# Kernel tuning notes

Hardware: AMD Instinct MI355X
Metric: run time of the kernel (lower is better)

Reference implementation:

```python
import jax, jax.numpy as jnp
import numpy as np

B, R, T, D = 16, 1024, 512, 1024
H = 1024  # hidden_dim

def setup_inputs() -> dict:
    key = jax.random.key(0)
    ks = jax.random.split(key, 8)
    s_in = 1.0 / np.sqrt(D)
    s_comb = 1.0 / np.sqrt(3 * D)
    return {
        "region_feats": jax.random.normal(ks[0], (B, R, D), jnp.float32),
        "query_embs": jax.random.normal(ks[1], (B, T, D), jnp.float32),
        "Wr": jax.random.normal(ks[2], (D, H), jnp.float32) * s_in,
        "br": jnp.zeros((H,), jnp.float32),
        "Wq": jax.random.normal(ks[3], (D, H), jnp.float32) * s_in,
        "bq": jnp.zeros((H,), jnp.float32),
        "Ws": jax.random.normal(ks[4], (3 * D, 1), jnp.float32) * s_comb,
        "bs": jnp.zeros((1,), jnp.float32),
    }

def reference(region_feats, query_embs, Wr, br, Wq, bq, Ws, bs):
    # Dense projections
    R_proj = region_feats @ Wr + br            # [B,R,H]
    Q_proj = query_embs @ Wq + bq              # [B,T,H]
    # Unscaled cross-attention scores
    scores = jnp.einsum('brd,btd->brt', R_proj, Q_proj)  # [B,R,T]
    attn = jax.nn.softmax(scores, axis=-1)
    # Attend over RAW query embeddings (as in source)
    attended = jnp.einsum('brt,btd->brd', attn, query_embs)  # [B,R,D]
    combined = jnp.concatenate(
        [region_feats, attended, region_feats * attended], axis=-1)  # [B,R,3D]
    out = combined @ Ws + bs                    # [B,R,1]
    return jnp.squeeze(out, axis=-1)            # [B,R]
```

## Files before the change

kernel.cpp:

```cpp
#include <hip/hip_runtime.h>


#define BD 16
#define RD 1024
#define TD 512
#define DD 1024
#define BR (BD * RD)

typedef _Float16 half8 __attribute__((ext_vector_type(8)));
typedef _Float16 half4 __attribute__((ext_vector_type(4)));
typedef float floatx4 __attribute__((ext_vector_type(4)));

__device__ __forceinline__ float wave_sum(float v) {
#pragma unroll
  for (int off = 32; off > 0; off >>= 1) v += __shfl_down(v, off);
  return v;
}

template <bool FUSED>
__global__ __launch_bounds__(256) void gemm_pipe(
    const _Float16* __restrict__ A, const _Float16* __restrict__ B0,
    const _Float16* __restrict__ B1, _Float16* __restrict__ C,
    float* __restrict__ Ms, float* __restrict__ Ls, float* __restrict__ Hs,
    const float* __restrict__ cvec, const _Float16* __restrict__ wsh,
    int N, int K, long sA, long sB, long sC) {
  constexpr int TT = FUSED ? 3 : 2;
  __shared__ __align__(16) _Float16 lds[2 * TT * 4096];
  __shared__ __align__(16) _Float16 wlds[FUSED ? 2048 : 16];

  const int b = blockIdx.z;
  A += (long)b * sA;
  B0 += (long)b * sB;
  if (FUSED) B1 += (long)b * sB;
  const int m0 = blockIdx.y * 128, n0 = blockIdx.x * 128;
  const int tid = threadIdx.x, lane = tid & 63, w = tid >> 6;
  const int wr = w >> 1, wc = w & 1;

  const int srow = lane >> 2;
  const int slot = lane & 3;
  const int scol = (slot ^ ((srow >> 1) & 3)) * 8;
  const _Float16* gA = A + (long)(m0 + 32 * w + srow) * K + scol;
  const _Float16* gP = B0 + (long)(n0 + 32 * w + srow) * K + scol;
  const _Float16* gQ = FUSED ? B1 + (long)(n0 + 32 * w + srow) * K + scol : nullptr;
  const long rstep = (long)16 * K;
  const int wofs = (32 * w + srow) * 32 + slot * 8;

  if (FUSED) *(int4*)&wlds[tid * 8] = *(const int4*)&wsh[tid * 8];

  const int NK = K / 32;
  int4 pA0, pA1, pP0, pP1, pQ0, pQ1;
  pA0 = *(const int4*)gA;
  pA1 = *(const int4*)(gA + rstep);
  pP0 = *(const int4*)gP;
  pP1 = *(const int4*)(gP + rstep);
  if (FUSED) {
    pQ0 = *(const int4*)gQ;
    pQ1 = *(const int4*)(gQ + rstep);
  }
  *(int4*)&lds[wofs] = pA0;
  *(int4*)&lds[wofs + 512] = pA1;
  *(int4*)&lds[4096 + wofs] = pP0;
  *(int4*)&lds[4096 + wofs + 512] = pP1;
  if (FUSED) {
    *(int4*)&lds[8192 + wofs] = pQ0;
    *(int4*)&lds[8192 + wofs + 512] = pQ1;
  }
  if (NK > 1) {
    pA0 = *(const int4*)(gA + 32);
    pA1 = *(const int4*)(gA + rstep + 32);
    pP0 = *(const int4*)(gP + 32);
    pP1 = *(const int4*)(gP + rstep + 32);
    if (FUSED) {
      pQ0 = *(const int4*)(gQ + 32);
      pQ1 = *(const int4*)(gQ + rstep + 32);
    }
  }
  __syncthreads();

  floatx4 accS[4][4] = {};
  floatx4 accH[4][4] = {};
  const int fr = lane & 15, g = lane >> 4;
  const int fs = (g ^ ((fr >> 1) & 3)) * 8;

  for (int kt = 0; kt < NK; ++kt) {
    const int cur = (kt & 1) * TT * 4096;
    const int nxt = ((kt + 1) & 1) * TT * 4096;
    if (kt + 1 < NK) {
      *(int4*)&lds[nxt + wofs] = pA0;
      *(int4*)&lds[nxt + wofs + 512] = pA1;
      *(int4*)&lds[nxt + 4096 + wofs] = pP0;
      *(int4*)&lds[nxt + 4096 + wofs + 512] = pP1;
      if (FUSED) {
        *(int4*)&lds[nxt + 8192 + wofs] = pQ0;
        *(int4*)&lds[nxt + 8192 + wofs + 512] = pQ1;
      }
    }
    if (kt + 2 < NK) {
      const long go = (long)(kt + 2) * 32;
      pA0 = *(const int4*)(gA + go);
      pA1 = *(const int4*)(gA + rstep + go);
      pP0 = *(const int4*)(gP + go);
      pP1 = *(const int4*)(gP + rstep + go);
      if (FUSED) {
        pQ0 = *(const int4*)(gQ + go);
        pQ1 = *(const int4*)(gQ + rstep + go);
      }
    }
    half8 af[4], bp[4], bq[4], w1f, w2f;
#pragma unroll
    for (int i = 0; i < 4; ++i)
      af[i] = *(const half8*)&lds[cur + (64 * wr + 16 * i + fr) * 32 + fs];
#pragma unroll
    for (int j = 0; j < 4; ++j)
      bp[j] = *(const half8*)&lds[cur + 4096 + (64 * wc + 16 * j + fr) * 32 + fs];
    if (FUSED) {
#pragma unroll
      for (int j = 0; j < 4; ++j)
        bq[j] = *(const half8*)&lds[cur + 8192 + (64 * wc + 16 * j + fr) * 32 + fs];
      w1f = *(const half8*)&wlds[kt * 32 + g * 8];
      w2f = *(const half8*)&wlds[1024 + kt * 32 + g * 8];
    }
#pragma unroll
    for (int i = 0; i < 4; ++i)
#pragma unroll
      for (int j = 0; j < 4; ++j)
        accS[i][j] = __builtin_amdgcn_mfma_f32_16x16x32_f16(af[i], bp[j], accS[i][j], 0, 0, 0);
    if (FUSED) {
#pragma unroll
      for (int i = 0; i < 4; ++i) af[i] = w1f + af[i] * w2f;
#pragma unroll
      for (int i = 0; i < 4; ++i)
#pragma unroll
        for (int j = 0; j < 4; ++j)
          accH[i][j] = __builtin_amdgcn_mfma_f32_16x16x32_f16(af[i], bq[j], accH[i][j], 0, 0, 0);
    }
    __syncthreads();
  }

  const int cr = g * 4, cc = fr;
  if (!FUSED) {
    _Float16* Cw = C + (long)b * sC;
#pragma unroll
    for (int i = 0; i < 4; ++i)
#pragma unroll
      for (int r = 0; r < 4; ++r)
#pragma unroll
        for (int j = 0; j < 4; ++j)
          Cw[(long)(m0 + 64 * wr + 16 * i + cr + r) * N + n0 + 64 * wc + 16 * j + cc] =
              (_Float16)accS[i][j][r];
  } else {
    float cv[4];
#pragma unroll
    for (int j = 0; j < 4; ++j)
      cv[j] = cvec[(long)b * TD + n0 + 64 * wc + 16 * j + cc];
    const int chunk = blockIdx.x * 2 + wc;
    const long rowBase = (long)b * RD + m0 + 64 * wr + cr;
#pragma unroll
    for (int i = 0; i < 4; ++i) {
#pragma unroll
      for (int r = 0; r < 4; ++r) {
        float mx = -1e30f;
#pragma unroll
        for (int j = 0; j < 4; ++j) mx = fmaxf(mx, accS[i][j][r] + cv[j]);
        mx = fmaxf(mx, __shfl_xor(mx, 1));
        mx = fmaxf(mx, __shfl_xor(mx, 2));
        mx = fmaxf(mx, __shfl_xor(mx, 4));
        mx = fmaxf(mx, __shfl_xor(mx, 8));
        float l = 0.f, hs = 0.f;
#pragma unroll
        for (int j = 0; j < 4; ++j) {
          const float e = __expf(accS[i][j][r] + cv[j] - mx);
          l += e;
          hs += e * accH[i][j][r];
        }
        l += __shfl_xor(l, 1); hs += __shfl_xor(hs, 1);
        l += __shfl_xor(l, 2); hs += __shfl_xor(hs, 2);
        l += __shfl_xor(l, 4); hs += __shfl_xor(hs, 4);
        l += __shfl_xor(l, 8); hs += __shfl_xor(hs, 8);
        if (cc == 0) {
          const long idx = (long)chunk * BR + rowBase + 16 * i + r;
          Ms[idx] = mx;
          Ls[idx] = l;
          Hs[idx] = hs;
        }
      }
    }
  }
}

__global__ __launch_bounds__(256) void combine(
    const float* __restrict__ Ms, const float* __restrict__ Ls,
    const float* __restrict__ Hs, const float* __restrict__ rdvec,
    const float* __restrict__ bs, float* __restrict__ out) {
  const int row = blockIdx.x * 256 + threadIdx.x;
  float mv[8];
  float gm = -1e30f;
#pragma unroll
  for (int c = 0; c < 8; ++c) {
    mv[c] = Ms[(long)c * BR + row];
    gm = fmaxf(gm, mv[c]);
  }
  float L = 0.f, HS = 0.f;
#pragma unroll
  for (int c = 0; c < 8; ++c) {
    const float s = __expf(mv[c] - gm);
    L += Ls[(long)c * BR + row] * s;
    HS += Hs[(long)c * BR + row] * s;
  }
  out[row] = HS / L + rdvec[row] + bs[0];
}

__global__ __launch_bounds__(256) void cvt_f2h(const float* __restrict__ in,
                                               _Float16* __restrict__ out) {
  const long i = ((long)blockIdx.x * 256 + threadIdx.x) * 4;
  const float4 v = *(const float4*)&in[i];
  half4 h = {(_Float16)v.x, (_Float16)v.y, (_Float16)v.z, (_Float16)v.w};
  *(half4*)&out[i] = h;
}

__global__ __launch_bounds__(256) void conv_region(
    const float* __restrict__ region, const float* __restrict__ Ws,
    _Float16* __restrict__ r16, float* __restrict__ rdvec) {
  const long row = blockIdx.x;
  const int tid = threadIdx.x, lane = tid & 63, wid = tid >> 6;
  const long i = row * DD + tid * 4;
  const float4 v = *(const float4*)&region[i];
  half4 h = {(_Float16)v.x, (_Float16)v.y, (_Float16)v.z, (_Float16)v.w};
  *(half4*)&r16[i] = h;
  const float4 w0 = *(const float4*)&Ws[tid * 4];
  float rd = v.x * w0.x + v.y * w0.y + v.z * w0.z + v.w * w0.w;
  rd = wave_sum(rd);
  __shared__ float sm[4];
  if (lane == 0) sm[wid] = rd;
  __syncthreads();
  if (tid == 0) rdvec[row] = sm[0] + sm[1] + sm[2] + sm[3];
}

__global__ __launch_bounds__(256) void conv_query(
    const float* __restrict__ query, const float* __restrict__ wqbr,
    _Float16* __restrict__ q16, float* __restrict__ cvec) {
  const long row = blockIdx.x;
  const int tid = threadIdx.x, lane = tid & 63, wid = tid >> 6;
  const long i = row * DD + tid * 4;
  const float4 v = *(const float4*)&query[i];
  half4 h = {(_Float16)v.x, (_Float16)v.y, (_Float16)v.z, (_Float16)v.w};
  *(half4*)&q16[i] = h;
  const float4 w = *(const float4*)&wqbr[tid * 4];
  float c = v.x * w.x + v.y * w.y + v.z * w.z + v.w * w.w;
  c = wave_sum(c);
  __shared__ float sm[4];
  if (lane == 0) sm[wid] = c;
  __syncthreads();
  if (tid == 0) cvec[row] = sm[0] + sm[1] + sm[2] + sm[3];
}

__global__ __launch_bounds__(256) void rowdot(const float* __restrict__ X,
                                              const float* __restrict__ v,
                                              float* __restrict__ outv, int Kk) {
  const int row = blockIdx.x * 4 + (threadIdx.x >> 6);
  const int lane = threadIdx.x & 63;
  const float* x = X + (long)row * Kk;
  float s = 0.f;
  for (int k = lane; k < Kk; k += 64) s += x[k] * v[k];
  s = wave_sum(s);
  if (lane == 0) outv[row] = s;
}

extern "C" void kernel_launch(void* const* d_in, const int* in_sizes, int n_in,
                              void* d_out, int out_size, void* d_ws, size_t ws_size,
                              hipStream_t stream) {
  const float* region = (const float*)d_in[0];
  const float* query  = (const float*)d_in[1];
  const float* Wr     = (const float*)d_in[2];
  const float* br     = (const float*)d_in[3];
  const float* Wq     = (const float*)d_in[4];
  const float* Ws     = (const float*)d_in[6];
  const float* bs     = (const float*)d_in[7];
  float* out = (float*)d_out;

  char* p = (char*)d_ws;
  _Float16* region16 = (_Float16*)p;
  _Float16* query16  = (_Float16*)(p + (32u << 20));
  _Float16* Qp       = (_Float16*)(p + (48u << 20));
  _Float16* Wr16     = (_Float16*)(p + (64u << 20));
  _Float16* Wq16     = (_Float16*)(p + (66u << 20));
  _Float16* M2       = (_Float16*)(p + (68u << 20));
  _Float16* Ws16     = (_Float16*)(p + (70u << 20));
  float*    wqbr     = (float*)(p + (70u << 20) + 65536);
  float*    cvec     = wqbr + 1024;
  float*    rdvec    = cvec + BD * TD;
  float*    Ms       = (float*)(p + (72u << 20));
  float*    Ls       = Ms + 8 * BR;
  float*    Hs       = Ls + 8 * BR;

  cvt_f2h<<<dim3(1024), 256, 0, stream>>>(Wr, Wr16);
  cvt_f2h<<<dim3(1024), 256, 0, stream>>>(Wq, Wq16);
  cvt_f2h<<<dim3(2), 256, 0, stream>>>(Ws + DD, Ws16);
  rowdot<<<dim3(DD / 4), 256, 0, stream>>>(Wq, br, wqbr, DD);
  conv_region<<<dim3(BD * RD), 256, 0, stream>>>(region, Ws, region16, rdvec);
  conv_query<<<dim3(BD * TD), 256, 0, stream>>>(query, wqbr, query16, cvec);

  gemm_pipe<false><<<dim3(8, 8, 1), 256, 0, stream>>>(
      Wr16, Wq16, nullptr, M2, nullptr, nullptr, nullptr, nullptr, nullptr,
      DD, DD, 0, 0, 0);
  gemm_pipe<false><<<dim3(8, 64, 1), 256, 0, stream>>>(
      query16, M2, nullptr, Qp, nullptr, nullptr, nullptr, nullptr, nullptr,
      DD, DD, 0, 0, 0);
  gemm_pipe<true><<<dim3(TD / 128, RD / 128, BD), 256, 0, stream>>>(
      region16, Qp, query16, nullptr, Ms, Ls, Hs, cvec, Ws16,
      TD, DD, (long)RD * DD, (long)TD * DD, 0);
  combine<<<dim3(BR / 256), 256, 0, stream>>>(Ms, Ls, Hs, rdvec, bs, out);
}
```

Before: 259.4 us.

## Use 512-thread GEMM blocks, remap block IDs for locality, merge prep kernels

The GEMM kernels move from 4 to 8 waves per 128x128 tile. Each wave now computes a 32x128 slice, so per-thread accumulators and staging registers are halved, and launch bounds allow 4 blocks per CU. A linear block-index remap groups tiles (XCD-style interleave via lin&7) to improve L2 locality across dies for the projection and fused attention GEMMs. The weight conversions and the Wq·br rowdot are merged into one prep kernel to cut launch count. The cost is that each wave reuses fewer B fragments per A fragment, and every tile now needs more waves and barriers.

```diff
diff --git a/kernel.cpp b/kernel.cpp
--- a/kernel.cpp
+++ b/kernel.cpp
@@ -18,67 +18,66 @@
 }
 
 template <bool FUSED>
-__global__ __launch_bounds__(256) void gemm_pipe(
+__global__ __launch_bounds__(512, 4) void gemm_pipe(
     const _Float16* __restrict__ A, const _Float16* __restrict__ B0,
     const _Float16* __restrict__ B1, _Float16* __restrict__ C,
     float* __restrict__ Ms, float* __restrict__ Ls, float* __restrict__ Hs,
     const float* __restrict__ cvec, const _Float16* __restrict__ wsh,
-    int N, int K, long sA, long sB, long sC) {
+    int N, int K, long sA, long sB, long sC, int remap) {
   constexpr int TT = FUSED ? 3 : 2;
   __shared__ __align__(16) _Float16 lds[2 * TT * 4096];
   __shared__ __align__(16) _Float16 wlds[FUSED ? 2048 : 16];
 
-  const int b = blockIdx.z;
+  const int lin = blockIdx.x + gridDim.x * (blockIdx.y + gridDim.y * blockIdx.z);
+  int b, mt, nt;
+  if (remap == 2) {
+    const int s = lin & 7, u = lin >> 3;
+    b = 2 * s + (u >> 5);
+    const int t = u & 31;
+    mt = t >> 2; nt = t & 3;
+  } else if (remap == 1) {
+    const int s = lin & 7, u = lin >> 3;
+    b = 0;
+    mt = s * 8 + (u >> 3); nt = u & 7;
+  } else {
+    b = blockIdx.z; mt = blockIdx.y; nt = blockIdx.x;
+  }
+  const int m0 = mt * 128, n0 = nt * 128;
   A += (long)b * sA;
   B0 += (long)b * sB;
   if (FUSED) B1 += (long)b * sB;
-  const int m0 = blockIdx.y * 128, n0 = blockIdx.x * 128;
+
   const int tid = threadIdx.x, lane = tid & 63, w = tid >> 6;
   const int wr = w >> 1, wc = w & 1;
 
-  const int srow = lane >> 2;
+  const int lrow = lane >> 2;
   const int slot = lane & 3;
-  const int scol = (slot ^ ((srow >> 1) & 3)) * 8;
-  const _Float16* gA = A + (long)(m0 + 32 * w + srow) * K + scol;
-  const _Float16* gP = B0 + (long)(n0 + 32 * w + srow) * K + scol;
-  const _Float16* gQ = FUSED ? B1 + (long)(n0 + 32 * w + srow) * K + scol : nullptr;
-  const long rstep = (long)16 * K;
-  const int wofs = (32 * w + srow) * 32 + slot * 8;
-
-  if (FUSED) *(int4*)&wlds[tid * 8] = *(const int4*)&wsh[tid * 8];
+  const int scol = (slot ^ ((lrow >> 1) & 3)) * 8;
+  const int srow = 16 * w + lrow;
+  const _Float16* gA = A + (long)(m0 + srow) * K + scol;
+  const _Float16* gP = B0 + (long)(n0 + srow) * K + scol;
+  const _Float16* gQ = FUSED ? B1 + (long)(n0 + srow) * K + scol : nullptr;
+  const int wofs = srow * 32 + slot * 8;
+
+  if (FUSED && tid < 256) *(int4*)&wlds[tid * 8] = *(const int4*)&wsh[tid * 8];
 
   const int NK = K / 32;
-  int4 pA0, pA1, pP0, pP1, pQ0, pQ1;
-  pA0 = *(const int4*)gA;
-  pA1 = *(const int4*)(gA + rstep);
-  pP0 = *(const int4*)gP;
-  pP1 = *(const int4*)(gP + rstep);
-  if (FUSED) {
-    pQ0 = *(const int4*)gQ;
-    pQ1 = *(const int4*)(gQ + rstep);
-  }
-  *(int4*)&lds[wofs] = pA0;
-  *(int4*)&lds[wofs + 512] = pA1;
-  *(int4*)&lds[4096 + wofs] = pP0;
-  *(int4*)&lds[4096 + wofs + 512] = pP1;
-  if (FUSED) {
-    *(int4*)&lds[8192 + wofs] = pQ0;
-    *(int4*)&lds[8192 + wofs + 512] = pQ1;
-  }
+  int4 pA, pP, pQ;
+  pA = *(const int4*)gA;
+  pP = *(const int4*)gP;
+  if (FUSED) pQ = *(const int4*)gQ;
+  *(int4*)&lds[wofs] = pA;
+  *(int4*)&lds[4096 + wofs] = pP;
+  if (FUSED) *(int4*)&lds[8192 + wofs] = pQ;
   if (NK > 1) {
-    pA0 = *(const int4*)(gA + 32);
-    pA1 = *(const int4*)(gA + rstep + 32);
-    pP0 = *(const int4*)(gP + 32);
-    pP1 = *(const int4*)(gP + rstep + 32);
-    if (FUSED) {
-      pQ0 = *(const int4*)(gQ + 32);
-      pQ1 = *(const int4*)(gQ + rstep + 32);
-    }
+    pA = *(const int4*)(gA + 32);
+    pP = *(const int4*)(gP + 32);
+    if (FUSED) pQ = *(const int4*)(gQ + 32);
   }
   __syncthreads();
 
-  floatx4 accS[4][4] = {};
-  floatx4 accH[4][4] = {};
+  floatx4 accS[2][4] = {};
+  floatx4 accH[2][4] = {};
   const int fr = lane & 15, g = lane >> 4;
   const int fs = (g ^ ((fr >> 1) & 3)) * 8;
 
@@ -86,30 +85,20 @@
     const int cur = (kt & 1) * TT * 4096;
     const int nxt = ((kt + 1) & 1) * TT * 4096;
     if (kt + 1 < NK) {
-      *(int4*)&lds[nxt + wofs] = pA0;
-      *(int4*)&lds[nxt + wofs + 512] = pA1;
-      *(int4*)&lds[nxt + 4096 + wofs] = pP0;
-      *(int4*)&lds[nxt + 4096 + wofs + 512] = pP1;
-      if (FUSED) {
-        *(int4*)&lds[nxt + 8192 + wofs] = pQ0;
-        *(int4*)&lds[nxt + 8192 + wofs + 512] = pQ1;
-      }
+      *(int4*)&lds[nxt + wofs] = pA;
+      *(int4*)&lds[nxt + 4096 + wofs] = pP;
+      if (FUSED) *(int4*)&lds[nxt + 8192 + wofs] = pQ;
     }
     if (kt + 2 < NK) {
       const long go = (long)(kt + 2) * 32;
-      pA0 = *(const int4*)(gA + go);
-      pA1 = *(const int4*)(gA + rstep + go);
-      pP0 = *(const int4*)(gP + go);
-      pP1 = *(const int4*)(gP + rstep + go);
-      if (FUSED) {
-        pQ0 = *(const int4*)(gQ + go);
-        pQ1 = *(const int4*)(gQ + rstep + go);
-      }
-    }
-    half8 af[4], bp[4], bq[4], w1f, w2f;
-#pragma unroll
-    for (int i = 0; i < 4; ++i)
-      af[i] = *(const half8*)&lds[cur + (64 * wr + 16 * i + fr) * 32 + fs];
+      pA = *(const int4*)(gA + go);
+      pP = *(const int4*)(gP + go);
+      if (FUSED) pQ = *(const int4*)(gQ + go);
+    }
+    half8 af[2], bp[4], bq[4], w1f, w2f;
+#pragma unroll
+    for (int i = 0; i < 2; ++i)
+      af[i] = *(const half8*)&lds[cur + (32 * wr + 16 * i + fr) * 32 + fs];
 #pragma unroll
     for (int j = 0; j < 4; ++j)
       bp[j] = *(const half8*)&lds[cur + 4096 + (64 * wc + 16 * j + fr) * 32 + fs];
@@ -121,15 +110,15 @@
       w2f = *(const half8*)&wlds[1024 + kt * 32 + g * 8];
     }
 #pragma unroll
-    for (int i = 0; i < 4; ++i)
+    for (int i = 0; i < 2; ++i)
 #pragma unroll
       for (int j = 0; j < 4; ++j)
         accS[i][j] = __builtin_amdgcn_mfma_f32_16x16x32_f16(af[i], bp[j], accS[i][j], 0, 0, 0);
     if (FUSED) {
 #pragma unroll
-      for (int i = 0; i < 4; ++i) af[i] = w1f + af[i] * w2f;
-#pragma unroll
-      for (int i = 0; i < 4; ++i)
+      for (int i = 0; i < 2; ++i) af[i] = w1f + af[i] * w2f;
+#pragma unroll
+      for (int i = 0; i < 2; ++i)
 #pragma unroll
         for (int j = 0; j < 4; ++j)
           accH[i][j] = __builtin_amdgcn_mfma_f32_16x16x32_f16(af[i], bq[j], accH[i][j], 0, 0, 0);
@@ -141,22 +130,22 @@
   if (!FUSED) {
     _Float16* Cw = C + (long)b * sC;
 #pragma unroll
-    for (int i = 0; i < 4; ++i)
+    for (int i = 0; i < 2; ++i)
 #pragma unroll
       for (int r = 0; r < 4; ++r)
 #pragma unroll
         for (int j = 0; j < 4; ++j)
-          Cw[(long)(m0 + 64 * wr + 16 * i + cr + r) * N + n0 + 64 * wc + 16 * j + cc] =
+          Cw[(long)(m0 + 32 * wr + 16 * i + cr + r) * N + n0 + 64 * wc + 16 * j + cc] =
               (_Float16)accS[i][j][r];
   } else {
     float cv[4];
 #pragma unroll
     for (int j = 0; j < 4; ++j)
       cv[j] = cvec[(long)b * TD + n0 + 64 * wc + 16 * j + cc];
-    const int chunk = blockIdx.x * 2 + wc;
-    const long rowBase = (long)b * RD + m0 + 64 * wr + cr;
-#pragma unroll
-    for (int i = 0; i < 4; ++i) {
+    const int chunk = nt * 2 + wc;
+    const long rowBase = (long)b * RD + m0 + 32 * wr + cr;
+#pragma unroll
+    for (int i = 0; i < 2; ++i) {
 #pragma unroll
       for (int r = 0; r < 4; ++r) {
         float mx = -1e30f;
@@ -210,12 +199,31 @@
   out[row] = HS / L + rdvec[row] + bs[0];
 }
 
-__global__ __launch_bounds__(256) void cvt_f2h(const float* __restrict__ in,
-                                               _Float16* __restrict__ out) {
-  const long i = ((long)blockIdx.x * 256 + threadIdx.x) * 4;
-  const float4 v = *(const float4*)&in[i];
-  half4 h = {(_Float16)v.x, (_Float16)v.y, (_Float16)v.z, (_Float16)v.w};
-  *(half4*)&out[i] = h;
+__global__ __launch_bounds__(256) void prep(
+    const float* __restrict__ Wr, const float* __restrict__ Wq,
+    const float* __restrict__ Ws, const float* __restrict__ br,
+    _Float16* __restrict__ Wr16, _Float16* __restrict__ Wq16,
+    _Float16* __restrict__ Ws16, float* __restrict__ wqbr) {
+  const int blk = blockIdx.x, tid = threadIdx.x;
+  if (blk < 2050) {
+    const float* src;
+    _Float16* dst;
+    long i;
+    if (blk < 1024) { src = Wr; dst = Wr16; i = (long)blk * 1024 + tid * 4; }
+    else if (blk < 2048) { src = Wq; dst = Wq16; i = (long)(blk - 1024) * 1024 + tid * 4; }
+    else { src = Ws + DD; dst = Ws16; i = (long)(blk - 2048) * 1024 + tid * 4; }
+    const float4 v = *(const float4*)&src[i];
+    half4 h = {(_Float16)v.x, (_Float16)v.y, (_Float16)v.z, (_Float16)v.w};
+    *(half4*)&dst[i] = h;
+  } else {
+    const int row = (blk - 2050) * 4 + (tid >> 6);
+    const int lane = tid & 63;
+    const float* x = Wq + (long)row * DD;
+    float s = 0.f;
+    for (int k = lane; k < DD; k += 64) s += x[k] * br[k];
+    s = wave_sum(s);
+    if (lane == 0) wqbr[row] = s;
+  }
 }
 
 __global__ __launch_bounds__(256) void conv_region(
@@ -254,18 +262,6 @@
   if (tid == 0) cvec[row] = sm[0] + sm[1] + sm[2] + sm[3];
 }
 
-__global__ __launch_bounds__(256) void rowdot(const float* __restrict__ X,
-                                              const float* __restrict__ v,
-                                              float* __restrict__ outv, int Kk) {
-  const int row = blockIdx.x * 4 + (threadIdx.x >> 6);
-  const int lane = threadIdx.x & 63;
-  const float* x = X + (long)row * Kk;
-  float s = 0.f;
-  for (int k = lane; k < Kk; k += 64) s += x[k] * v[k];
-  s = wave_sum(s);
-  if (lane == 0) outv[row] = s;
-}
-
 extern "C" void kernel_launch(void* const* d_in, const int* in_sizes, int n_in,
                               void* d_out, int out_size, void* d_ws, size_t ws_size,
                               hipStream_t stream) {
@@ -293,21 +289,18 @@
   float*    Ls       = Ms + 8 * BR;
   float*    Hs       = Ls + 8 * BR;
 
-  cvt_f2h<<<dim3(1024), 256, 0, stream>>>(Wr, Wr16);
-  cvt_f2h<<<dim3(1024), 256, 0, stream>>>(Wq, Wq16);
-  cvt_f2h<<<dim3(2), 256, 0, stream>>>(Ws + DD, Ws16);
-  rowdot<<<dim3(DD / 4), 256, 0, stream>>>(Wq, br, wqbr, DD);
+  prep<<<dim3(2306), 256, 0, stream>>>(Wr, Wq, Ws, br, Wr16, Wq16, Ws16, wqbr);
   conv_region<<<dim3(BD * RD), 256, 0, stream>>>(region, Ws, region16, rdvec);
   conv_query<<<dim3(BD * TD), 256, 0, stream>>>(query, wqbr, query16, cvec);
 
-  gemm_pipe<false><<<dim3(8, 8, 1), 256, 0, stream>>>(
+  gemm_pipe<false><<<dim3(8, 8, 1), 512, 0, stream>>>(
       Wr16, Wq16, nullptr, M2, nullptr, nullptr, nullptr, nullptr, nullptr,
-      DD, DD, 0, 0, 0);
-  gemm_pipe<false><<<dim3(8, 64, 1), 256, 0, stream>>>(
+      DD, DD, 0, 0, 0, 0);
+  gemm_pipe<false><<<dim3(8, 64, 1), 512, 0, stream>>>(
       query16, M2, nullptr, Qp, nullptr, nullptr, nullptr, nullptr, nullptr,
-      DD, DD, 0, 0, 0);
-  gemm_pipe<true><<<dim3(TD / 128, RD / 128, BD), 256, 0, stream>>>(
+      DD, DD, 0, 0, 0, 1);
+  gemm_pipe<true><<<dim3(TD / 128, RD / 128, BD), 512, 0, stream>>>(
       region16, Qp, query16, nullptr, Ms, Ls, Hs, cvec, Ws16,
-      TD, DD, (long)RD * DD, (long)TD * DD, 0);
+      TD, DD, (long)RD * DD, (long)TD * DD, 0, 2);
   combine<<<dim3(BR / 256), 256, 0, stream>>>(Ms, Ls, Hs, rdvec, bs, out);
 }
```

Result: faster. 229.3 us (-11.6%).
